# Kernel tuning notes

Hardware: AMD Instinct MI355X
Metric: run time of the kernel (lower is better)

## Reference

```python
import jax, jax.numpy as jnp
import numpy as np

PAD = 4
B, C, H, W = 64, 9, 256, 256


def setup_inputs() -> dict:
    key = jax.random.key(0)
    k1, k2, k3 = jax.random.split(key, 3)
    x = jax.random.normal(k1, (B, C, H, W), dtype=jnp.float32)
    shift_x = jax.random.randint(k2, (B,), 0, 2 * PAD + 1, dtype=jnp.int32)
    shift_y = jax.random.randint(k3, (B,), 0, 2 * PAD + 1, dtype=jnp.int32)
    return {"x": x, "shift_x": shift_x, "shift_y": shift_y}


def _lerp_gather(xp, idx_f, axis_size, axis):
    """Separable bilinear tap along one spatial axis with zeros padding.

    xp: (B, C, D2, D3); idx_f: (B, L) fractional pixel indices along `axis`.
    Returns gathered+interpolated tensor with that axis resized to L.
    """
    i0 = jnp.floor(idx_f)
    w1 = idx_f - i0
    w0 = 1.0 - w1
    i1 = i0 + 1.0

    def tap(i, w):
        valid = (i >= 0) & (i <= axis_size - 1)  # zeros padding_mode
        ic = jnp.clip(i, 0, axis_size - 1).astype(jnp.int32)
        wm = w * valid
        if axis == 3:
            g = jnp.take_along_axis(xp, ic[:, None, None, :], axis=3)
            return g * wm[:, None, None, :]
        else:
            g = jnp.take_along_axis(xp, ic[:, None, :, None], axis=2)
            return g * wm[:, None, :, None]

    return tap(i0, w0) + tap(i1, w1)


def reference(x, shift_x, shift_y):
    b, c, h, w = x.shape
    p = PAD
    hp, wp = h + 2 * p, w + 2 * p
    # replicate pad
    x_pad = jnp.pad(x, ((0, 0), (0, 0), (p, p), (p, p)), mode='edge')
    # base grid (normalized coords, H/W points spanning [-1+eps, 1-eps])
    eps_h, eps_w = 2.0 / hp, 2.0 / wp
    gy = jnp.linspace(-1.0 + eps_h, 1.0 - eps_h, h).astype(x.dtype)  # (H,)
    gx = jnp.linspace(-1.0 + eps_w, 1.0 - eps_w, w).astype(x.dtype)  # (W,)
    # per-sample integer-pixel shift in normalized units
    gxb = gx[None, :] + shift_x.astype(x.dtype)[:, None] * (2.0 / wp)  # (B,W)
    gyb = gy[None, :] + shift_y.astype(x.dtype)[:, None] * (2.0 / hp)  # (B,H)
    # normalized -> pixel coords (align_corners=False)
    ix = ((gxb + 1.0) * wp - 1.0) * 0.5  # (B,W)
    iy = ((gyb + 1.0) * hp - 1.0) * 0.5  # (B,H)
    # separable bilinear grid_sample with zeros padding
    tmp = _lerp_gather(x_pad, ix, wp, axis=3)  # (B,C,Hp,W)
    out = _lerp_gather(tmp, iy, hp, axis=2)    # (B,C,H,W)
    return out
```

## Files before the change

### kernel.cpp

```cpp
#include <hip/hip_runtime.h>

#define PAD 4
#define B_ 64
#define C_ 9
#define H_ 256
#define W_ 256
#define PEXT 264
#define TILE_R 16
#define SROWS 18
#define LROW 268

__global__ __launch_bounds__(256) void RandomShiftsAug_kernel(
    const float* __restrict__ x,
    const int* __restrict__ shift_x,
    const int* __restrict__ shift_y,
    float* __restrict__ out)
{
    __shared__ float sm[SROWS * LROW];

    const int tid  = threadIdx.x;
    const int lane = tid & 63;
    const int wv   = tid >> 6;

    const int bc   = blockIdx.x >> 4;
    const int rblk = blockIdx.x & 15;
    const int i0   = rblk << 4;
    const int b    = bc / C_;

    const float STEP = 262.0f / 255.0f;
    const float sx = (float)shift_x[b];
    const float sy = (float)shift_y[b];
    const float xbase = 0.5f + sx;
    const float ybase = 0.5f + sy;

    const int sr_base = (int)floorf(fmaf((float)i0, STEP, ybase));

    const float* __restrict__ plane = x + (size_t)bc * (size_t)(H_ * W_);

    for (int s = wv; s < SROWS; s += 4) {
        const int rs = min(max(sr_base + s - PAD, 0), H_ - 1);
        const float* src = plane + rs * W_ + lane * 4;
        float* dst = &sm[s * LROW + 4];
        __builtin_amdgcn_global_load_lds(
            (const __attribute__((address_space(1))) void*)src,
            (__attribute__((address_space(3))) void*)dst,
            16, 0, 0);
    }
    __syncthreads();

    if (tid < SROWS * 9) {
        const int s = tid / 9;
        const int e = tid - s * 9;
        const int p    = (e < 4) ? e : (256 + e);
        const int srcd = (e < 4) ? 4 : 259;
        sm[s * LROW + p] = sm[s * LROW + srcd];
    }
    __syncthreads();

    float wx0[4], wx1[4];
    int rdc[4];
    #pragma unroll
    for (int c = 0; c < 4; ++c) {
        const int j   = lane + 64 * c;
        const float ixv = fmaf((float)j, STEP, xbase);
        const float fx  = floorf(ixv);
        const int   px0 = (int)fx;
        float w1 = ixv - fx;
        float w0 = 1.0f - w1;
        if (px0 > PEXT - 1)     w0 = 0.0f;
        if (px0 + 1 > PEXT - 1) w1 = 0.0f;
        wx0[c] = w0;
        wx1[c] = w1;
        rdc[c] = min(px0, PEXT - 1);
    }

    #pragma unroll
    for (int m = 0; m < 4; ++m) {
        const int i = i0 + wv * 4 + m;
        const float iyv = fmaf((float)i, STEP, ybase);
        const float fy  = floorf(iyv);
        const int   py0 = (int)fy;
        float wy1 = iyv - fy;
        float wy0 = 1.0f - wy1;
        if (py0 > PEXT - 1)     wy0 = 0.0f;
        if (py0 + 1 > PEXT - 1) wy1 = 0.0f;
        const int s0 = py0 - sr_base;
        const float* __restrict__ r0p = &sm[s0 * LROW];
        const float* __restrict__ r1p = r0p + LROW;
        float* __restrict__ orow = out + ((size_t)(bc * H_ + i)) * (size_t)W_;

        #pragma unroll
        for (int c = 0; c < 4; ++c) {
            const int rd = rdc[c];
            const float v00 = r0p[rd], v01 = r0p[rd + 1];
            const float v10 = r1p[rd], v11 = r1p[rd + 1];
            const float a0 = fmaf(v00, wx0[c], v01 * wx1[c]);
            const float a1 = fmaf(v10, wx0[c], v11 * wx1[c]);
            orow[lane + 64 * c] = fmaf(a0, wy0, a1 * wy1);
        }
    }
}

extern "C" void kernel_launch(void* const* d_in, const int* in_sizes, int n_in,
                              void* d_out, int out_size, void* d_ws, size_t ws_size,
                              hipStream_t stream) {
    const float* x       = (const float*)d_in[0];
    const int*   shift_x = (const int*)d_in[1];
    const int*   shift_y = (const int*)d_in[2];
    float*       out     = (float*)d_out;

    const int blocks = B_ * C_ * (H_ / TILE_R);
    RandomShiftsAug_kernel<<<blocks, 256, 0, stream>>>(x, shift_x, shift_y, out);
}
```

Measured before the change: 54.47 us.

## Double-buffer two row tiles per block and fold horizontal edge padding into weights

Each block of 512 threads now handles 32 output rows as two 16-row halves. The second half's rows are staged into a separate LDS buffer while the first half is computed, which overlaps the global-to-LDS copy with compute. Replicate padding on the x axis is folded into the bilinear weights, so the LDS fix-up pass and its barrier are gone, and only the source rows actually needed are loaded. Block indices are also remapped to interleave work across the grid. The block is larger and uses twice the LDS, which may lower occupancy.

```diff
diff --git a/kernel.cpp b/kernel.cpp
--- a/kernel.cpp
+++ b/kernel.cpp
@@ -6,25 +6,26 @@
 #define H_ 256
 #define W_ 256
 #define PEXT 264
-#define TILE_R 16
+#define HTILE 16
 #define SROWS 18
-#define LROW 268
+#define NBLK (B_ * C_ * (H_ / 32))
 
-__global__ __launch_bounds__(256) void RandomShiftsAug_kernel(
+__global__ __launch_bounds__(512, 8) void RandomShiftsAug_kernel(
     const float* __restrict__ x,
     const int* __restrict__ shift_x,
     const int* __restrict__ shift_y,
     float* __restrict__ out)
 {
-    __shared__ float sm[SROWS * LROW];
+    __shared__ float sm[2][SROWS][W_];
 
     const int tid  = threadIdx.x;
     const int lane = tid & 63;
     const int wv   = tid >> 6;
 
-    const int bc   = blockIdx.x >> 4;
-    const int rblk = blockIdx.x & 15;
-    const int i0   = rblk << 4;
+    const int wid  = (blockIdx.x & 7) * (NBLK / 8) + (blockIdx.x >> 3);
+
+    const int bc   = wid >> 3;
+    const int I0   = (wid & 7) << 5;
     const int b    = bc / C_;
 
     const float STEP = 262.0f / 255.0f;
@@ -33,35 +34,23 @@
     const float xbase = 0.5f + sx;
     const float ybase = 0.5f + sy;
 
-    const int sr_base = (int)floorf(fmaf((float)i0, STEP, ybase));
-
     const float* __restrict__ plane = x + (size_t)bc * (size_t)(H_ * W_);
 
-    for (int s = wv; s < SROWS; s += 4) {
-        const int rs = min(max(sr_base + s - PAD, 0), H_ - 1);
-        const float* src = plane + rs * W_ + lane * 4;
-        float* dst = &sm[s * LROW + 4];
-        __builtin_amdgcn_global_load_lds(
-            (const __attribute__((address_space(1))) void*)src,
-            (__attribute__((address_space(3))) void*)dst,
-            16, 0, 0);
+    int srb[2], srn[2];
+    #pragma unroll
+    for (int h = 0; h < 2; ++h) {
+        const int i0 = I0 + h * HTILE;
+        const int lo = (int)floorf(fmaf((float)i0, STEP, ybase));
+        const int hi = (int)floorf(fmaf((float)(i0 + HTILE - 1), STEP, ybase)) + 1;
+        srb[h] = lo;
+        srn[h] = hi - lo + 1;
     }
-    __syncthreads();
-
-    if (tid < SROWS * 9) {
-        const int s = tid / 9;
-        const int e = tid - s * 9;
-        const int p    = (e < 4) ? e : (256 + e);
-        const int srcd = (e < 4) ? 4 : 259;
-        sm[s * LROW + p] = sm[s * LROW + srcd];
-    }
-    __syncthreads();
 
     float wx0[4], wx1[4];
-    int rdc[4];
+    int cx[4];
     #pragma unroll
     for (int c = 0; c < 4; ++c) {
-        const int j   = lane + 64 * c;
+        const int j = lane + 64 * c;
         const float ixv = fmaf((float)j, STEP, xbase);
         const float fx  = floorf(ixv);
         const int   px0 = (int)fx;
@@ -69,36 +58,62 @@
         float w0 = 1.0f - w1;
         if (px0 > PEXT - 1)     w0 = 0.0f;
         if (px0 + 1 > PEXT - 1) w1 = 0.0f;
+        const int s = px0 - PAD;
+        if (s < 0)    { w0 += w1; w1 = 0.0f; }
+        if (s >= 255) { w1 += w0; w0 = 0.0f; }
+        cx[c]  = min(max(s, 0), 254);
         wx0[c] = w0;
         wx1[c] = w1;
-        rdc[c] = min(px0, PEXT - 1);
     }
 
-    #pragma unroll
-    for (int m = 0; m < 4; ++m) {
-        const int i = i0 + wv * 4 + m;
-        const float iyv = fmaf((float)i, STEP, ybase);
-        const float fy  = floorf(iyv);
-        const int   py0 = (int)fy;
-        float wy1 = iyv - fy;
-        float wy0 = 1.0f - wy1;
-        if (py0 > PEXT - 1)     wy0 = 0.0f;
-        if (py0 + 1 > PEXT - 1) wy1 = 0.0f;
-        const int s0 = py0 - sr_base;
-        const float* __restrict__ r0p = &sm[s0 * LROW];
-        const float* __restrict__ r1p = r0p + LROW;
-        float* __restrict__ orow = out + ((size_t)(bc * H_ + i)) * (size_t)W_;
+    auto stage = [&](int h) {
+        const int base = srb[h];
+        const int n    = srn[h];
+        for (int s = wv; s < n; s += 8) {
+            const int rs = min(max(base + s - PAD, 0), H_ - 1);
+            const float* src = plane + rs * W_ + lane * 4;
+            __builtin_amdgcn_global_load_lds(
+                (const __attribute__((address_space(1))) void*)src,
+                (__attribute__((address_space(3))) void*)&sm[h][s][0],
+                16, 0, 0);
+        }
+    };
 
+    auto compute = [&](int h) {
+        const int i0 = I0 + h * HTILE;
         #pragma unroll
-        for (int c = 0; c < 4; ++c) {
-            const int rd = rdc[c];
-            const float v00 = r0p[rd], v01 = r0p[rd + 1];
-            const float v10 = r1p[rd], v11 = r1p[rd + 1];
-            const float a0 = fmaf(v00, wx0[c], v01 * wx1[c]);
-            const float a1 = fmaf(v10, wx0[c], v11 * wx1[c]);
-            orow[lane + 64 * c] = fmaf(a0, wy0, a1 * wy1);
+        for (int m = 0; m < 2; ++m) {
+            const int i = i0 + wv * 2 + m;
+            const float iyv = fmaf((float)i, STEP, ybase);
+            const float fy  = floorf(iyv);
+            const int   py0 = (int)fy;
+            float wy1 = iyv - fy;
+            float wy0 = 1.0f - wy1;
+            if (py0 > PEXT - 1)     wy0 = 0.0f;
+            if (py0 + 1 > PEXT - 1) wy1 = 0.0f;
+            const int s0 = py0 - srb[h];
+            const float* __restrict__ r0p = &sm[h][s0][0];
+            const float* __restrict__ r1p = &sm[h][s0 + 1][0];
+            float* __restrict__ orow = out + ((size_t)(bc * H_ + i)) * (size_t)W_;
+
+            #pragma unroll
+            for (int c = 0; c < 4; ++c) {
+                const int rd = cx[c];
+                const float v00 = r0p[rd], v01 = r0p[rd + 1];
+                const float v10 = r1p[rd], v11 = r1p[rd + 1];
+                const float a0 = fmaf(v00, wx0[c], v01 * wx1[c]);
+                const float a1 = fmaf(v10, wx0[c], v11 * wx1[c]);
+                orow[lane + 64 * c] = fmaf(a0, wy0, a1 * wy1);
+            }
         }
-    }
+    };
+
+    stage(0);
+    __syncthreads();
+    stage(1);
+    compute(0);
+    __syncthreads();
+    compute(1);
 }
 
 extern "C" void kernel_launch(void* const* d_in, const int* in_sizes, int n_in,
@@ -109,6 +124,5 @@
     const int*   shift_y = (const int*)d_in[2];
     float*       out     = (float*)d_out;
 
-    const int blocks = B_ * C_ * (H_ / TILE_R);
-    RandomShiftsAug_kernel<<<blocks, 256, 0, stream>>>(x, shift_x, shift_y, out);
+    RandomShiftsAug_kernel<<<NBLK, 512, 0, stream>>>(x, shift_x, shift_y, out);
 }
```

New measurement: 52.69 us. -3.3%, faster.
